# Kernel tuning notes

Measured on AMD Instinct MI355X. Metric: run time of the kernel, lower is better.

Reference implementation:

```python
import jax, jax.numpy as jnp
import numpy as np
import math

H = 8          # n_head
MAX_POS = 48   # block_size / max_positions
MAX_PART = 16  # max_particles


def _rel_bias(table, L, max_len):
    # table: (2*max_len-1, H). Equivalent to the tile/view trick in
    # SimpleRelativePositionalBias: bias[h, i, j] = b[j - i + L - 1, h]
    b = table[max_len - L: max_len + L - 1]          # (2L-1, H)
    idx = jnp.arange(L)
    rel = idx[None, :] - idx[:, None] + (L - 1)      # (L, L) in [0, 2L-2]
    return jnp.transpose(b[rel], (2, 0, 1))          # (H, L, L)


def setup_inputs() -> dict:
    key = jax.random.key(0)
    ks = jax.random.split(key, 7)
    B, N, T, C = 16, 16, 48, 512
    s = 0.02
    return {
        "x": jax.random.normal(ks[0], (B, N, T, C), jnp.float32),
        "Wq": jax.random.normal(ks[1], (C, C), jnp.float32) * s,
        "Wk": jax.random.normal(ks[2], (C, C), jnp.float32) * s,
        "Wv": jax.random.normal(ks[3], (C, C), jnp.float32) * s,
        "Wo": jax.random.normal(ks[4], (C, C), jnp.float32) * s,
        "rel_pos_bias": jax.random.normal(ks[5], (2 * MAX_POS - 1, H), jnp.float32) * s,
        "particle_rel_pos_bias": jax.random.normal(ks[6], (2 * MAX_PART - 1, H), jnp.float32) * s,
    }


def reference(x, Wq, Wk, Wv, Wo, rel_pos_bias, particle_rel_pos_bias):
    B, N, T, C = x.shape
    hd = C // H
    L = N * T
    xf = x.reshape(B, L, C)
    # (B, H, L, hd) each; Linear with no bias
    q = (xf @ Wq).reshape(B, L, H, hd).transpose(0, 2, 1, 3)
    k = (xf @ Wk).reshape(B, L, H, hd).transpose(0, 2, 1, 3)
    v = (xf @ Wv).reshape(B, L, H, hd).transpose(0, 2, 1, 3)

    att = jnp.einsum('bhqd,bhkd->bhqk', q, k) * (1.0 / math.sqrt(hd))
    att = att.reshape(B, H, N, T, N, T)

    bias_t = _rel_bias(rel_pos_bias, T, MAX_POS).reshape(1, H, 1, T, 1, T)
    bias_p = _rel_bias(particle_rel_pos_bias, N, MAX_PART).reshape(1, H, N, 1, N, 1)
    att = att + bias_t + bias_p

    # causal over the time axes only (all particles at allowed times visible)
    causal = jnp.tril(jnp.ones((T, T), dtype=bool))
    att = jnp.where(causal[None, None, None, :, None, :], att, -jnp.inf)

    att = jax.nn.softmax(att.reshape(B, H, L, L), axis=-1)
    y = att @ v                                      # (B, H, L, hd)
    y = y.transpose(0, 2, 1, 3).reshape(B, L, C) @ Wo
    return y.reshape(B, N, T, C)
```

## Files before the change

kernel.cpp:

```cpp
#include <hip/hip_runtime.h>
#include <hip/hip_bf16.h>
#include <math.h>

#define B_  16
#define N_  16
#define T_  48
#define C_  512
#define H_  8
#define HD_ 64
#define L_  768
#define BL_ 12288

typedef __attribute__((ext_vector_type(8))) short b16x8;
typedef __attribute__((ext_vector_type(4))) float f32x4;
typedef __attribute__((ext_vector_type(2))) unsigned int u32x2;

__device__ __forceinline__ short f2b(float f) {
  __hip_bfloat16 h = __float2bfloat16(f);
  return *reinterpret_cast<short*>(&h);
}
__device__ __forceinline__ unsigned cvt_pk_bf16(float a, float b) {
  unsigned d;
  asm("v_cvt_pk_bf16_f32 %0, %1, %2" : "=v"(d) : "v"(a), "v"(b));
  return d;
}
__device__ __forceinline__ float ex2(float x) {
  float d;
  asm("v_exp_f32 %0, %1" : "=v"(d) : "v"(x));
  return d;
}
__device__ __forceinline__ void gload16(const void* g, void* l) {
  __builtin_amdgcn_global_load_lds(
      (const __attribute__((address_space(1))) void*)g,
      (__attribute__((address_space(3))) void*)l, 16, 0, 0);
}

__global__ __launch_bounds__(256) void prep_kernel(
    const float* __restrict__ x,
    const float* __restrict__ Wq, const float* __restrict__ Wk,
    const float* __restrict__ Wv, const float* __restrict__ Wo,
    short* __restrict__ xb, short* __restrict__ WT)
{
  __shared__ float tile[32][33];
  int blk = blockIdx.x;
  int tid = threadIdx.x;
  if (blk < 3072) {
    int i = blk * 256 + tid;
    const float4* src = (const float4*)(x + (size_t)i * 8);
    float4 a = src[0], b = src[1];
    short tmp[8] = {f2b(a.x), f2b(a.y), f2b(a.z), f2b(a.w),
                    f2b(b.x), f2b(b.y), f2b(b.z), f2b(b.w)};
    *(b16x8*)(xb + (size_t)i * 8) = *(b16x8*)tmp;
  } else {
    int idx = blk - 3072;
    int mat = idx >> 8, rem = idx & 255;
    const float* W = (mat == 0) ? Wq : (mat == 1) ? Wk : (mat == 2) ? Wv : Wo;
    float scale = (mat == 0) ? 0.18033688f : 1.0f;
    int k0 = (rem >> 4) * 32, n0 = (rem & 15) * 32;
    int tx = tid & 31, ty = tid >> 5;
    for (int i = ty; i < 32; i += 8) tile[i][tx] = W[(size_t)(k0 + i) * 512 + n0 + tx];
    __syncthreads();
    short* dst = WT + (size_t)mat * 262144;
    for (int i = ty; i < 32; i += 8)
      dst[(size_t)(n0 + i) * 512 + k0 + tx] = f2b(tile[tx][i] * scale);
  }
}

__global__ __launch_bounds__(256) void qkv_kernel(
    const short* __restrict__ xb, const short* __restrict__ WT,
    short* __restrict__ q2, short* __restrict__ k2, short* __restrict__ vT2)
{
  __shared__ __align__(16) short smem[16384];
  int tid = threadIdx.x;
  int w = tid >> 6, lane = tid & 63, n16 = lane & 15, quad = lane >> 4;
  int bm = blockIdx.x, bn = blockIdx.y;
  int mat = bn >> 2;
  int ncol0 = (bn & 3) * 128;
  const short* Wt = WT + (size_t)mat * 262144;
  int bq = bm / 6;
  int rr0 = (bm % 6) * 128;

  f32x4 zero4 = {0.f, 0.f, 0.f, 0.f};
  f32x4 acc[4][4];
  #pragma unroll
  for (int mt = 0; mt < 4; ++mt)
    #pragma unroll
    for (int nt = 0; nt < 4; ++nt) acc[mt][nt] = zero4;

  const short* gA[2];
  const short* gB[2];
  #pragma unroll
  for (int i = 0; i < 2; ++i) {
    int r16 = w + 4 * i;
    int rr = rr0 + r16 * 16 + (lane >> 2);
    int pt = rr >> 4, pn = rr & 15;
    gA[i] = xb + ((size_t)bq * 768 + pn * 48 + pt) * 512 + (lane & 3) * 8;
    gB[i] = Wt + (size_t)(ncol0 + r16 * 16 + (lane >> 2)) * 512 + (lane & 3) * 8;
  }
  int ldsoff = (w) * 512 + lane * 8;

  auto stage = [&](int buf, int kt) {
    short* As = smem + buf * 8192;
    short* Bs = As + 4096;
    #pragma unroll
    for (int i = 0; i < 2; ++i) {
      gload16(gA[i] + kt * 32, As + i * 2048 + ldsoff);
      gload16(gB[i] + kt * 32, Bs + i * 2048 + ldsoff);
    }
  };

  int wm = (w >> 1) * 64, wn = (w & 1) * 64;
  stage(0, 0);
  __syncthreads();
  int buf = 0;
  for (int kt = 0; kt < 16; ++kt) {
    if (kt < 15) stage(buf ^ 1, kt + 1);
    const short (*As)[32] = (const short(*)[32])(smem + buf * 8192);
    const short (*Bs)[32] = (const short(*)[32])(smem + buf * 8192 + 4096);
    b16x8 af[4], bf[4];
    #pragma unroll
    for (int mt = 0; mt < 4; ++mt) af[mt] = *(const b16x8*)&As[wm + mt * 16 + n16][quad * 8];
    #pragma unroll
    for (int nt = 0; nt < 4; ++nt) bf[nt] = *(const b16x8*)&Bs[wn + nt * 16 + n16][quad * 8];
    #pragma unroll
    for (int mt = 0; mt < 4; ++mt)
      #pragma unroll
      for (int nt = 0; nt < 4; ++nt)
        acc[mt][nt] = __builtin_amdgcn_mfma_f32_16x16x32_bf16(af[mt], bf[nt], acc[mt][nt], 0, 0, 0);
    __syncthreads();
    buf ^= 1;
  }

  short (*Ls)[136] = (short(*)[136])smem;
  for (int c = 0; c < 4; ++c) {
    __syncthreads();
    if ((w >> 1) == (c >> 1)) {
      int mtb = (c & 1) * 2;
      #pragma unroll
      for (int mi = 0; mi < 2; ++mi) {
        #pragma unroll
        for (int nt = 0; nt < 4; ++nt)
          #pragma unroll
          for (int r = 0; r < 4; ++r)
            Ls[mi * 16 + quad * 4 + r][wn + nt * 16 + n16] = f2b(acc[mtb + mi][nt][r]);
      }
    }
    __syncthreads();
    int rrc = rr0 + c * 32;
    if (mat != 2) {
      short* dst = (mat == 0) ? q2 : k2;
      int row = tid >> 3, c0 = (tid & 7) * 16;
      int hhg = (ncol0 + c0) >> 6, d0 = (ncol0 + c0) & 63;
      short* dp = dst + ((size_t)(bq * 8 + hhg) * 768 + rrc + row) * 64 + d0;
      *(b16x8*)dp       = *(b16x8*)&Ls[row][c0];
      *(b16x8*)(dp + 8) = *(b16x8*)&Ls[row][c0 + 8];
    } else {
      int cp = tid & 63, r8 = (tid >> 6) * 8;
      int c0 = 2 * cp;
      int hhg = (ncol0 + c0) >> 6, d0 = (ncol0 + c0) & 63;
      short t0[8], t1[8];
      #pragma unroll
      for (int j = 0; j < 8; ++j) { t0[j] = Ls[r8 + j][c0]; t1[j] = Ls[r8 + j][c0 + 1]; }
      short* dp = vT2 + ((size_t)(bq * 8 + hhg) * 64 + d0) * 768 + rrc + r8;
      *(b16x8*)dp         = *(b16x8*)t0;
      *(b16x8*)(dp + 768) = *(b16x8*)t1;
    }
  }
}

__global__ __launch_bounds__(128, 3) void attn_kernel(
    const short* __restrict__ q2, const short* __restrict__ k2,
    const short* __restrict__ vT2,
    const float* __restrict__ relT, const float* __restrict__ relP,
    short* __restrict__ yatt)
{
  __shared__ float btL[2][96];

  const float LOG2E = 1.44269504f;
  int tid = threadIdx.x;
  int wv = tid >> 6, lane = tid & 63, n16 = lane & 15, quad = lane >> 4;
  int blk = blockIdx.x;
  int h = blk & 7;
  int g = blk >> 3;
  int pg = g % 12, b = g / 12;
  int pair = pg * 2 + wv;
  int qtA = pair, qtB = 47 - pair;
  int nA = (qtA + 2) >> 1, nB = (qtB + 2) >> 1;

  btL[wv][lane] = relT[(lane < 95 ? lane : 94) * 8 + h] * LOG2E;
  if (lane < 32) btL[wv][64 + lane] = relT[((64 + lane) < 95 ? 64 + lane : 94) * 8 + h] * LOG2E;

  float bpT[4];
  #pragma unroll
  for (int r = 0; r < 4; ++r)
    bpT[r] = relP[(quad * 4 + r - n16 + 15) * 8 + h] * LOG2E;

  size_t bh = (size_t)(b * 8 + h);
  const short* qb = q2 + bh * 49152;
  const short* kb = k2 + bh * 49152;
  const short* vb = vT2 + bh * 49152;

  b16x8 qA0 = *(const b16x8*)(qb + (qtA * 16 + n16) * 64 + quad * 8);
  b16x8 qA1 = *(const b16x8*)(qb + (qtA * 16 + n16) * 64 + quad * 8 + 32);
  b16x8 qB0 = *(const b16x8*)(qb + (qtB * 16 + n16) * 64 + quad * 8);
  b16x8 qB1 = *(const b16x8*)(qb + (qtB * 16 + n16) * 64 + quad * 8 + 32);

  f32x4 zero4 = {0.f, 0.f, 0.f, 0.f};
  f32x4 oA[4], oB[4];
  float psA = 0.f, psB = 0.f;
  #pragma unroll
  for (int nt = 0; nt < 4; ++nt) { oA[nt] = zero4; oB[nt] = zero4; }

  b16x8 kfa[4], kfb[4], vfa[4], vfb[4];
  auto loadKV = [&](int kt2, b16x8* kf, b16x8* vf) {
    const short* kp = kb + (size_t)(kt2 * 32 + n16) * 64 + quad * 8;
    kf[0] = *(const b16x8*)kp;
    kf[1] = *(const b16x8*)(kp + 32);
    kf[2] = *(const b16x8*)(kp + 1024);
    kf[3] = *(const b16x8*)(kp + 1024 + 32);
    const short* vp = vb + (size_t)n16 * 768 + kt2 * 32 + quad * 8;
    vf[0] = *(const b16x8*)vp;
    vf[1] = *(const b16x8*)(vp + 16 * 768);
    vf[2] = *(const b16x8*)(vp + 32 * 768);
    vf[3] = *(const b16x8*)(vp + 48 * 768);
  };

  auto exp_pack = [&](const f32x4& s0, const f32x4& s1, float bt0, float bt1,
                      float& ps) -> b16x8 {
    float e00 = ex2(s0[0] + bt0 + bpT[0]);
    float e01 = ex2(s0[1] + bt0 + bpT[1]);
    float e02 = ex2(s0[2] + bt0 + bpT[2]);
    float e03 = ex2(s0[3] + bt0 + bpT[3]);
    float e10 = ex2(s1[0] + bt1 + bpT[0]);
    float e11 = ex2(s1[1] + bt1 + bpT[1]);
    float e12 = ex2(s1[2] + bt1 + bpT[2]);
    float e13 = ex2(s1[3] + bt1 + bpT[3]);
    ps += ((e00 + e01) + (e02 + e03)) + ((e10 + e11) + (e12 + e13));
    unsigned p0 = cvt_pk_bf16(e00, e01);
    unsigned p1 = cvt_pk_bf16(e02, e03);
    unsigned p2 = cvt_pk_bf16(e10, e11);
    unsigned p3 = cvt_pk_bf16(e12, e13);
    u32x2 a02 = __builtin_amdgcn_permlane32_swap(p0, p2, false, false);
    u32x2 z02 = __builtin_amdgcn_permlane16_swap(a02.x, a02.y, false, false);
    u32x2 a13 = __builtin_amdgcn_permlane32_swap(p1, p3, false, false);
    u32x2 z13 = __builtin_amdgcn_permlane16_swap(a13.x, a13.y, false, false);
    union { unsigned u[4]; b16x8 v; } r;
    r.u[0] = z02.x;
    r.u[1] = z13.x;
    r.u[2] = z02.y;
    r.u[3] = z13.y;
    return r.v;
  };

  auto step = [&](int kt2, const b16x8* kf, const b16x8* vf) {
    int kt0 = kt2 * 2;
    bool doA = kt2 < nA;
    f32x4 sB0 = zero4, sB1 = zero4;
    sB0 = __builtin_amdgcn_mfma_f32_16x16x32_bf16(kf[0], qB0, sB0, 0, 0, 0);
    sB0 = __builtin_amdgcn_mfma_f32_16x16x32_bf16(kf[1], qB1, sB0, 0, 0, 0);
    sB1 = __builtin_amdgcn_mfma_f32_16x16x32_bf16(kf[2], qB0, sB1, 0, 0, 0);
    sB1 = __builtin_amdgcn_mfma_f32_16x16x32_bf16(kf[3], qB1, sB1, 0, 0, 0);
    f32x4 sA0 = zero4, sA1 = zero4;
    if (doA) {
      sA0 = __builtin_amdgcn_mfma_f32_16x16x32_bf16(kf[0], qA0, sA0, 0, 0, 0);
      sA0 = __builtin_amdgcn_mfma_f32_16x16x32_bf16(kf[1], qA1, sA0, 0, 0, 0);
      sA1 = __builtin_amdgcn_mfma_f32_16x16x32_bf16(kf[2], qA0, sA1, 0, 0, 0);
      sA1 = __builtin_amdgcn_mfma_f32_16x16x32_bf16(kf[3], qA1, sA1, 0, 0, 0);
    }
    float btB0 = (kt0 <= qtB) ? btL[wv][kt0 - qtB + 47] : -1e30f;
    float btB1 = (kt0 + 1 <= qtB) ? btL[wv][kt0 + 1 - qtB + 47] : -1e30f;
    b16x8 pfB = exp_pack(sB0, sB1, btB0, btB1, psB);
    #pragma unroll
    for (int nt = 0; nt < 4; ++nt)
      oB[nt] = __builtin_amdgcn_mfma_f32_16x16x32_bf16(pfB, vf[nt], oB[nt], 0, 0, 0);
    if (doA) {
      float btA0 = (kt0 <= qtA) ? btL[wv][kt0 - qtA + 47] : -1e30f;
      float btA1 = (kt0 + 1 <= qtA) ? btL[wv][kt0 + 1 - qtA + 47] : -1e30f;
      b16x8 pfA = exp_pack(sA0, sA1, btA0, btA1, psA);
      #pragma unroll
      for (int nt = 0; nt < 4; ++nt)
        oA[nt] = __builtin_amdgcn_mfma_f32_16x16x32_bf16(pfA, vf[nt], oA[nt], 0, 0, 0);
    }
  };

  loadKV(0, kfa, vfa);
  for (int kt2 = 0; kt2 < nB; kt2 += 2) {
    if (kt2 + 1 < nB) loadKV(kt2 + 1, kfb, vfb);
    step(kt2, kfa, vfa);
    if (kt2 + 1 < nB) {
      if (kt2 + 2 < nB) loadKV(kt2 + 2, kfa, vfa);
      step(kt2 + 1, kfb, vfb);
    }
  }

  psA += __shfl_xor(psA, 16); psA += __shfl_xor(psA, 32);
  psB += __shfl_xor(psB, 16); psB += __shfl_xor(psB, 32);
  float invA = 1.0f / psA, invB = 1.0f / psB;
  float pnA[4], pnB[4];
  #pragma unroll
  for (int r = 0; r < 4; ++r) {
    pnA[r] = __shfl(invA, quad * 4 + r);
    pnB[r] = __shfl(invB, quad * 4 + r);
  }

  #pragma unroll
  for (int nt = 0; nt < 4; ++nt) {
    int c = h * 64 + nt * 16 + n16;
    #pragma unroll
    for (int r = 0; r < 4; ++r) {
      int qn = quad * 4 + r;
      yatt[((size_t)b * 768 + qn * 48 + qtA) * 512 + c] = f2b(oA[nt][r] * pnA[r]);
      yatt[((size_t)b * 768 + qn * 48 + qtB) * 512 + c] = f2b(oB[nt][r] * pnB[r]);
    }
  }
}

__global__ __launch_bounds__(256) void proj_kernel(
    const short* __restrict__ yatt, const short* __restrict__ WT,
    float* __restrict__ out)
{
  __shared__ __align__(16) short smem[16384];
  int tid = threadIdx.x;
  int w = tid >> 6, lane = tid & 63, n16 = lane & 15, quad = lane >> 4;
  int row0 = blockIdx.x * 128;
  int ncol0 = blockIdx.y * 128;
  const short* Wt = WT + (size_t)3 * 262144;

  f32x4 zero4 = {0.f, 0.f, 0.f, 0.f};
  f32x4 acc[4][4];
  #pragma unroll
  for (int mt = 0; mt < 4; ++mt)
    #pragma unroll
    for (int nt = 0; nt < 4; ++nt) acc[mt][nt] = zero4;

  const short* gA[2];
  const short* gB[2];
  #pragma unroll
  for (int i = 0; i < 2; ++i) {
    int r16 = w + 4 * i;
    gA[i] = yatt + (size_t)(row0 + r16 * 16 + (lane >> 2)) * 512 + (lane & 3) * 8;
    gB[i] = Wt + (size_t)(ncol0 + r16 * 16 + (lane >> 2)) * 512 + (lane & 3) * 8;
  }
  int ldsoff = w * 512 + lane * 8;

  auto stage = [&](int buf, int kt) {
    short* As = smem + buf * 8192;
    short* Bs = As + 4096;
    #pragma unroll
    for (int i = 0; i < 2; ++i) {
      gload16(gA[i] + kt * 32, As + i * 2048 + ldsoff);
      gload16(gB[i] + kt * 32, Bs + i * 2048 + ldsoff);
    }
  };

  int wm = (w >> 1) * 64, wn = (w & 1) * 64;
  stage(0, 0);
  __syncthreads();
  int buf = 0;
  for (int kt = 0; kt < 16; ++kt) {
    if (kt < 15) stage(buf ^ 1, kt + 1);
    const short (*As)[32] = (const short(*)[32])(smem + buf * 8192);
    const short (*Bs)[32] = (const short(*)[32])(smem + buf * 8192 + 4096);
    b16x8 af[4], bf[4];
    #pragma unroll
    for (int mt = 0; mt < 4; ++mt) af[mt] = *(const b16x8*)&As[wm + mt * 16 + n16][quad * 8];
    #pragma unroll
    for (int nt = 0; nt < 4; ++nt) bf[nt] = *(const b16x8*)&Bs[wn + nt * 16 + n16][quad * 8];
    #pragma unroll
    for (int mt = 0; mt < 4; ++mt)
      #pragma unroll
      for (int nt = 0; nt < 4; ++nt)
        acc[mt][nt] = __builtin_amdgcn_mfma_f32_16x16x32_bf16(af[mt], bf[nt], acc[mt][nt], 0, 0, 0);
    __syncthreads();
    buf ^= 1;
  }

  #pragma unroll
  for (int mt = 0; mt < 4; ++mt) {
    int rowb = row0 + wm + mt * 16 + quad * 4;
    #pragma unroll
    for (int nt = 0; nt < 4; ++nt) {
      int colg = ncol0 + wn + nt * 16 + n16;
      #pragma unroll
      for (int r = 0; r < 4; ++r)
        out[(size_t)(rowb + r) * 512 + colg] = acc[mt][nt][r];
    }
  }
}

extern "C" void kernel_launch(void* const* d_in, const int* in_sizes, int n_in,
                              void* d_out, int out_size, void* d_ws, size_t ws_size,
                              hipStream_t stream) {
  const float* x    = (const float*)d_in[0];
  const float* Wq   = (const float*)d_in[1];
  const float* Wk   = (const float*)d_in[2];
  const float* Wv   = (const float*)d_in[3];
  const float* Wo   = (const float*)d_in[4];
  const float* relT = (const float*)d_in[5];
  const float* relP = (const float*)d_in[6];

  char* wsb = (char*)d_ws;
  const size_t SZ = (size_t)BL_ * C_ * 2;
  short* xb  = (short*)(wsb);
  short* WT  = (short*)(wsb + SZ);
  short* qb  = (short*)(wsb + SZ + 2097152);
  short* kb  = (short*)(wsb + 2 * SZ + 2097152);
  short* vTb = (short*)(wsb + 3 * SZ + 2097152);
  short* yat = (short*)(wsb + 4 * SZ + 2097152 + 4096);

  prep_kernel<<<dim3(4096), dim3(256), 0, stream>>>(x, Wq, Wk, Wv, Wo, xb, WT);
  qkv_kernel<<<dim3(96, 12), dim3(256), 0, stream>>>(xb, WT, qb, kb, vTb);
  attn_kernel<<<dim3(1536), dim3(128), 0, stream>>>(qb, kb, vTb, relT, relP, yat);
  proj_kernel<<<dim3(96, 4), dim3(256), 0, stream>>>(yat, WT, (float*)d_out);
}
```

Before: 192.1 us.

## Stage K/V tiles through double-buffered LDS shared by both waves

The two waves in each block previously each loaded the full K and V fragments from global memory into registers. Now the block loads each 32-key K/V tile cooperatively once, writes it into a double-buffered LDS area, and each wave reads its fragments from LDS. This halves global/L2 traffic per block and the per-thread load count. The cost is a block-wide barrier every iteration, which couples the two waves' loop counts (nA/nB now derived from pg, uniform across waves) and adds LDS traffic and possible bank conflicts.

```diff
diff --git a/kernel.cpp b/kernel.cpp
--- a/kernel.cpp
+++ b/kernel.cpp
@@ -174,6 +174,7 @@
     const float* __restrict__ relT, const float* __restrict__ relP,
     short* __restrict__ yatt)
 {
+  __shared__ __align__(16) short KV[2][4096];
   __shared__ float btL[2][96];
 
   const float LOG2E = 1.44269504f;
@@ -185,7 +186,8 @@
   int pg = g % 12, b = g / 12;
   int pair = pg * 2 + wv;
   int qtA = pair, qtB = 47 - pair;
-  int nA = (qtA + 2) >> 1, nB = (qtB + 2) >> 1;
+  int nA = pg + 1;
+  int nB = 24 - pg;
 
   btL[wv][lane] = relT[(lane < 95 ? lane : 94) * 8 + h] * LOG2E;
   if (lane < 32) btL[wv][64 + lane] = relT[((64 + lane) < 95 ? 64 + lane : 94) * 8 + h] * LOG2E;
@@ -211,30 +213,37 @@
   #pragma unroll
   for (int nt = 0; nt < 4; ++nt) { oA[nt] = zero4; oB[nt] = zero4; }
 
-  b16x8 kfa[4], kfb[4], vfa[4], vfb[4];
-  auto loadKV = [&](int kt2, b16x8* kf, b16x8* vf) {
-    const short* kp = kb + (size_t)(kt2 * 32 + n16) * 64 + quad * 8;
-    kf[0] = *(const b16x8*)kp;
-    kf[1] = *(const b16x8*)(kp + 32);
-    kf[2] = *(const b16x8*)(kp + 1024);
-    kf[3] = *(const b16x8*)(kp + 1024 + 32);
-    const short* vp = vb + (size_t)n16 * 768 + kt2 * 32 + quad * 8;
-    vf[0] = *(const b16x8*)vp;
-    vf[1] = *(const b16x8*)(vp + 16 * 768);
-    vf[2] = *(const b16x8*)(vp + 32 * 768);
-    vf[3] = *(const b16x8*)(vp + 48 * 768);
+  int krow = tid >> 3, kc8 = tid & 7;
+  int vd   = tid >> 2, vkc = tid & 3;
+  int kdst = (kc8 < 4 ? 0 : 1024) + krow * 32 + (kc8 & 3) * 8;
+  int vdst = 2048 + vd * 32 + vkc * 8;
+  b16x8 s0, s1, s2, s3;
+  auto LOADR = [&](int kt2) {
+    const short* kq = kb + (size_t)(kt2 * 32 + krow) * 64 + kc8 * 8;
+    s0 = *(const b16x8*)kq;
+    s1 = *(const b16x8*)(kq + 16 * 64);
+    const short* vq = vb + (size_t)vd * 768 + kt2 * 32 + vkc * 8;
+    s2 = *(const b16x8*)vq;
+    s3 = *(const b16x8*)(vq + (size_t)32 * 768);
   };
-
-  auto exp_pack = [&](const f32x4& s0, const f32x4& s1, float bt0, float bt1,
+  auto WRITE = [&](int buf) {
+    short* p = KV[buf];
+    *(b16x8*)(p + kdst)       = s0;
+    *(b16x8*)(p + kdst + 512) = s1;
+    *(b16x8*)(p + vdst)        = s2;
+    *(b16x8*)(p + vdst + 1024) = s3;
+  };
+
+  auto exp_pack = [&](const f32x4& s0v, const f32x4& s1v, float bt0, float bt1,
                       float& ps) -> b16x8 {
-    float e00 = ex2(s0[0] + bt0 + bpT[0]);
-    float e01 = ex2(s0[1] + bt0 + bpT[1]);
-    float e02 = ex2(s0[2] + bt0 + bpT[2]);
-    float e03 = ex2(s0[3] + bt0 + bpT[3]);
-    float e10 = ex2(s1[0] + bt1 + bpT[0]);
-    float e11 = ex2(s1[1] + bt1 + bpT[1]);
-    float e12 = ex2(s1[2] + bt1 + bpT[2]);
-    float e13 = ex2(s1[3] + bt1 + bpT[3]);
+    float e00 = ex2(s0v[0] + bt0 + bpT[0]);
+    float e01 = ex2(s0v[1] + bt0 + bpT[1]);
+    float e02 = ex2(s0v[2] + bt0 + bpT[2]);
+    float e03 = ex2(s0v[3] + bt0 + bpT[3]);
+    float e10 = ex2(s1v[0] + bt1 + bpT[0]);
+    float e11 = ex2(s1v[1] + bt1 + bpT[1]);
+    float e12 = ex2(s1v[2] + bt1 + bpT[2]);
+    float e13 = ex2(s1v[3] + bt1 + bpT[3]);
     ps += ((e00 + e01) + (e02 + e03)) + ((e10 + e11) + (e12 + e13));
     unsigned p0 = cvt_pk_bf16(e00, e01);
     unsigned p1 = cvt_pk_bf16(e02, e03);
@@ -252,45 +261,59 @@
     return r.v;
   };
 
-  auto step = [&](int kt2, const b16x8* kf, const b16x8* vf) {
+  LOADR(0);
+  WRITE(0);
+  __syncthreads();
+
+  int buf = 0;
+  for (int kt2 = 0; kt2 < nB; ++kt2) {
+    bool more = (kt2 + 1 < nB);
+    if (more) LOADR(kt2 + 1);
+
+    const short* p = KV[buf];
+    b16x8 kf0 = *(const b16x8*)(p + n16 * 32 + quad * 8);
+    b16x8 kf1 = *(const b16x8*)(p + 1024 + n16 * 32 + quad * 8);
+    b16x8 kf2 = *(const b16x8*)(p + (16 + n16) * 32 + quad * 8);
+    b16x8 kf3 = *(const b16x8*)(p + 1024 + (16 + n16) * 32 + quad * 8);
+    b16x8 vf0 = *(const b16x8*)(p + 2048 + n16 * 32 + quad * 8);
+    b16x8 vf1 = *(const b16x8*)(p + 2048 + (16 + n16) * 32 + quad * 8);
+    b16x8 vf2 = *(const b16x8*)(p + 2048 + (32 + n16) * 32 + quad * 8);
+    b16x8 vf3 = *(const b16x8*)(p + 2048 + (48 + n16) * 32 + quad * 8);
+
     int kt0 = kt2 * 2;
     bool doA = kt2 < nA;
     f32x4 sB0 = zero4, sB1 = zero4;
-    sB0 = __builtin_amdgcn_mfma_f32_16x16x32_bf16(kf[0], qB0, sB0, 0, 0, 0);
-    sB0 = __builtin_amdgcn_mfma_f32_16x16x32_bf16(kf[1], qB1, sB0, 0, 0, 0);
-    sB1 = __builtin_amdgcn_mfma_f32_16x16x32_bf16(kf[2], qB0, sB1, 0, 0, 0);
-    sB1 = __builtin_amdgcn_mfma_f32_16x16x32_bf16(kf[3], qB1, sB1, 0, 0, 0);
+    sB0 = __builtin_amdgcn_mfma_f32_16x16x32_bf16(kf0, qB0, sB0, 0, 0, 0);
+    sB0 = __builtin_amdgcn_mfma_f32_16x16x32_bf16(kf1, qB1, sB0, 0, 0, 0);
+    sB1 = __builtin_amdgcn_mfma_f32_16x16x32_bf16(kf2, qB0, sB1, 0, 0, 0);
+    sB1 = __builtin_amdgcn_mfma_f32_16x16x32_bf16(kf3, qB1, sB1, 0, 0, 0);
     f32x4 sA0 = zero4, sA1 = zero4;
     if (doA) {
-      sA0 = __builtin_amdgcn_mfma_f32_16x16x32_bf16(kf[0], qA0, sA0, 0, 0, 0);
-      sA0 = __builtin_amdgcn_mfma_f32_16x16x32_bf16(kf[1], qA1, sA0, 0, 0, 0);
-      sA1 = __builtin_amdgcn_mfma_f32_16x16x32_bf16(kf[2], qA0, sA1, 0, 0, 0);
-      sA1 = __builtin_amdgcn_mfma_f32_16x16x32_bf16(kf[3], qA1, sA1, 0, 0, 0);
+      sA0 = __builtin_amdgcn_mfma_f32_16x16x32_bf16(kf0, qA0, sA0, 0, 0, 0);
+      sA0 = __builtin_amdgcn_mfma_f32_16x16x32_bf16(kf1, qA1, sA0, 0, 0, 0);
+      sA1 = __builtin_amdgcn_mfma_f32_16x16x32_bf16(kf2, qA0, sA1, 0, 0, 0);
+      sA1 = __builtin_amdgcn_mfma_f32_16x16x32_bf16(kf3, qA1, sA1, 0, 0, 0);
     }
     float btB0 = (kt0 <= qtB) ? btL[wv][kt0 - qtB + 47] : -1e30f;
     float btB1 = (kt0 + 1 <= qtB) ? btL[wv][kt0 + 1 - qtB + 47] : -1e30f;
     b16x8 pfB = exp_pack(sB0, sB1, btB0, btB1, psB);
-    #pragma unroll
-    for (int nt = 0; nt < 4; ++nt)
-      oB[nt] = __builtin_amdgcn_mfma_f32_16x16x32_bf16(pfB, vf[nt], oB[nt], 0, 0, 0);
+    oB[0] = __builtin_amdgcn_mfma_f32_16x16x32_bf16(pfB, vf0, oB[0], 0, 0, 0);
+    oB[1] = __builtin_amdgcn_mfma_f32_16x16x32_bf16(pfB, vf1, oB[1], 0, 0, 0);
+    oB[2] = __builtin_amdgcn_mfma_f32_16x16x32_bf16(pfB, vf2, oB[2], 0, 0, 0);
+    oB[3] = __builtin_amdgcn_mfma_f32_16x16x32_bf16(pfB, vf3, oB[3], 0, 0, 0);
     if (doA) {
       float btA0 = (kt0 <= qtA) ? btL[wv][kt0 - qtA + 47] : -1e30f;
       float btA1 = (kt0 + 1 <= qtA) ? btL[wv][kt0 + 1 - qtA + 47] : -1e30f;
       b16x8 pfA = exp_pack(sA0, sA1, btA0, btA1, psA);
-      #pragma unroll
-      for (int nt = 0; nt < 4; ++nt)
-        oA[nt] = __builtin_amdgcn_mfma_f32_16x16x32_bf16(pfA, vf[nt], oA[nt], 0, 0, 0);
-    }
-  };
-
-  loadKV(0, kfa, vfa);
-  for (int kt2 = 0; kt2 < nB; kt2 += 2) {
-    if (kt2 + 1 < nB) loadKV(kt2 + 1, kfb, vfb);
-    step(kt2, kfa, vfa);
-    if (kt2 + 1 < nB) {
-      if (kt2 + 2 < nB) loadKV(kt2 + 2, kfa, vfa);
-      step(kt2 + 1, kfb, vfb);
-    }
+      oA[0] = __builtin_amdgcn_mfma_f32_16x16x32_bf16(pfA, vf0, oA[0], 0, 0, 0);
+      oA[1] = __builtin_amdgcn_mfma_f32_16x16x32_bf16(pfA, vf1, oA[1], 0, 0, 0);
+      oA[2] = __builtin_amdgcn_mfma_f32_16x16x32_bf16(pfA, vf2, oA[2], 0, 0, 0);
+      oA[3] = __builtin_amdgcn_mfma_f32_16x16x32_bf16(pfA, vf3, oA[3], 0, 0, 0);
+    }
+
+    if (more) WRITE(buf ^ 1);
+    __syncthreads();
+    buf ^= 1;
   }
 
   psA += __shfl_xor(psA, 16); psA += __shfl_xor(psA, 32);
```

Result: faster. 157.4 us (-18.1%).
